# Performance work log

Measured on AMD Instinct MI355X. Metric: run time of the kernel, lower is better.

## Reference

```python
import jax, jax.numpy as jnp
import numpy as np

_SHAPE = (4, 2, 8, 256, 513)  # N, 2(real/imag), C, T, F


def setup_inputs() -> dict:
    key = jax.random.key(0)
    k1, k2, k3 = jax.random.split(key, 3)
    return {
        "mixture": jax.random.normal(k1, _SHAPE, dtype=jnp.float32),
        "target": jax.random.normal(k2, _SHAPE, dtype=jnp.float32),
        "noise": jax.random.normal(k3, _SHAPE, dtype=jnp.float32),
        "ref_mic_idx": 0,
    }


def _to_complex(x):
    # (N, 2, C, T, F) real-imag stacked -> complex (N, C, T, F)
    return jax.lax.complex(x[:, 0], x[:, 1])


def _mean_spatial_cov(s):
    # s: complex (N, C, T, F) -> time-averaged covariance (N, F, C, C)
    N, C, T, F = s.shape
    sc = jnp.transpose(s, (0, 3, 2, 1))  # (N, F, T, C)
    # outer product V V^H summed over T, fused into one batched GEMM
    return jnp.einsum("nftc,nftd->nfcd", sc, jnp.conj(sc)) / T


def reference(mixture, target, noise, ref_mic_idx):
    y = _to_complex(mixture)  # (N, C, T, F)
    x = _to_complex(target)
    v = _to_complex(noise)
    N, C, T, F = y.shape

    phi_target = _mean_spatial_cov(x)  # (N, F, C, C)
    # diagonal loading: torch adds load to BOTH real and imag parts (RI dim broadcast)
    load = (0.001 / np.sqrt(2)) * (1.0 + 1.0j)
    phi_noise = _mean_spatial_cov(v) + jnp.asarray(load, dtype=y.dtype) * jnp.eye(C, dtype=y.dtype)

    G = jnp.linalg.inv(phi_noise) @ phi_target  # (N, F, C, C)
    l = jnp.trace(G, axis1=-2, axis2=-1)  # (N, F)
    # W = (1/l) * G @ e_ref  -> select column ref_mic_idx
    W = G[..., ref_mic_idx] / l[..., None]  # (N, F, C)

    # X_bf(n,t,f) = W^H y = sum_c conj(W)_{nfc} y_{nctf}
    X_bf = jnp.einsum("nfc,nctf->ntf", jnp.conj(W), y)  # (N, T, F)
    # restack real/imag and add singleton channel dim -> (N, 2, 1, T, F)
    out = jnp.stack([X_bf.real, X_bf.imag], axis=1)[:, :, None]
    return out
```

## Files before the change

### kernel.cpp

```cpp
#include <hip/hip_runtime.h>

#define Nn 4
#define Cc 8
#define Tt 256
#define Ff 513
#define TFs (Tt * Ff)
#define NCHUNK 32
#define TCHUNK (Tt / NCHUNK)
#define SLAB ((size_t)Ff * 72)

__global__ __launch_bounds__(64) void cov_partial(
    const float* __restrict__ target, const float* __restrict__ noise,
    float* __restrict__ partial)
{
    int f = blockIdx.x * 64 + threadIdx.x;
    if (f >= Ff) return;
    int n = blockIdx.y;
    int z = blockIdx.z;
    int inp = z & 1;
    int chunk = z >> 1;

    const float* src = inp ? noise : target;
    const float* bt = src + (size_t)n * 2 * Cc * TFs + (size_t)(chunk * TCHUNK) * Ff + f;

    float ar[36], ai[36];
#pragma unroll
    for (int p = 0; p < 36; ++p) { ar[p] = 0.f; ai[p] = 0.f; }

#pragma unroll 2
    for (int tt = 0; tt < TCHUNK; ++tt) {
        float re[8], im[8];
#pragma unroll
        for (int c = 0; c < 8; ++c) {
            re[c] = bt[(size_t)c * TFs];
            im[c] = bt[(size_t)(Cc + c) * TFs];
        }
        int p = 0;
#pragma unroll
        for (int a = 0; a < 8; ++a) {
#pragma unroll
            for (int b = a; b < 8; ++b, ++p) {
                ar[p] += re[a] * re[b] + im[a] * im[b];
                if (a != b)
                    ai[p] += im[a] * re[b] - re[a] * im[b];
            }
        }
        bt += Ff;
    }

    float* dst = partial + (((size_t)inp * Nn + n) * NCHUNK + chunk) * SLAB
                 + (size_t)f * 72;
#pragma unroll
    for (int j = 0; j < 18; ++j) {
        float4 v = make_float4(ar[2 * j], ai[2 * j], ar[2 * j + 1], ai[2 * j + 1]);
        *(float4*)(dst + 4 * j) = v;
    }
}

__global__ __launch_bounds__(64) void mvdr_weights(
    const float* __restrict__ partial, const int* __restrict__ ref_ptr,
    float2* __restrict__ wconj)
{
    int f = blockIdx.x;
    int n = blockIdx.y;
    int lane = threadIdx.x;

    int r = lane >> 3, c = lane & 7;
    int lo = r < c ? r : c, hi = r < c ? c : r;
    int p = lo * 8 - lo * (lo - 1) / 2 + (hi - lo);

    const float* pT = partial + ((size_t)(0 * Nn + n) * NCHUNK) * SLAB
                      + (size_t)f * 72 + 2 * p;
    const float* pN = partial + ((size_t)(1 * Nn + n) * NCHUNK) * SLAB
                      + (size_t)f * 72 + 2 * p;
    float2 sT = make_float2(0.f, 0.f), sN = make_float2(0.f, 0.f);
#pragma unroll
    for (int ch = 0; ch < NCHUNK; ++ch) {
        float2 vT = *(const float2*)(pT + ch * SLAB);
        float2 vN = *(const float2*)(pN + ch * SLAB);
        sT.x += vT.x; sT.y += vT.y;
        sN.x += vN.x; sN.y += vN.y;
    }

    const float invT = 1.0f / (float)Tt;
    const float dl = 0.001f / 1.41421356237309515f;
    float sgn = (r > c) ? -1.f : 1.f;

    float2 a = make_float2(sN.x * invT, sgn * sN.y * invT);
    float2 b = make_float2(sT.x * invT, sgn * sT.y * invT);
    if (r == c) { a.x += dl; a.y += dl; }

    for (int k = 0; k < 8; ++k) {
        float mag = (c == k && r >= k) ? (a.x * a.x + a.y * a.y) : -1.f;
        int midx = r;
#pragma unroll
        for (int st = 8; st < 64; st <<= 1) {
            float om = __shfl_xor(mag, st, 64);
            int   oi = __shfl_xor(midx, st, 64);
            if (om > mag) { mag = om; midx = oi; }
        }
        int piv = __shfl(midx, k, 64);

        int srcr = (r == k) ? piv : ((r == piv) ? k : r);
        int src = srcr * 8 + c;
        a.x = __shfl(a.x, src, 64); a.y = __shfl(a.y, src, 64);
        b.x = __shfl(b.x, src, 64); b.y = __shfl(b.y, src, 64);

        float pvx = __shfl(a.x, k * 8 + k, 64), pvy = __shfl(a.y, k * 8 + k, 64);
        float d = pvx * pvx + pvy * pvy;
        float ipx = pvx / d, ipy = -pvy / d;
        if (r == k) {
            float2 t = a;
            a = make_float2(t.x * ipx - t.y * ipy, t.x * ipy + t.y * ipx);
            t = b;
            b = make_float2(t.x * ipx - t.y * ipy, t.x * ipy + t.y * ipx);
        }

        float rax = __shfl(a.x, k * 8 + c, 64), ray = __shfl(a.y, k * 8 + c, 64);
        float rbx = __shfl(b.x, k * 8 + c, 64), rby = __shfl(b.y, k * 8 + c, 64);
        float fx  = __shfl(a.x, r * 8 + k, 64), fy  = __shfl(a.y, r * 8 + k, 64);
        if (r != k) {
            a.x -= fx * rax - fy * ray;  a.y -= fx * ray + fy * rax;
            b.x -= fx * rbx - fy * rby;  b.y -= fx * rby + fy * rbx;
        }
    }

    float tx = (r == c) ? b.x : 0.f, ty = (r == c) ? b.y : 0.f;
#pragma unroll
    for (int st = 1; st < 64; st <<= 1) {
        tx += __shfl_xor(tx, st, 64);
        ty += __shfl_xor(ty, st, 64);
    }

    int ref = *ref_ptr;
    if (c == ref) {
        float den = tx * tx + ty * ty;
        float wx = (b.x * tx + b.y * ty) / den;
        float wy = (b.y * tx - b.x * ty) / den;
        wconj[((size_t)n * Ff + f) * 8 + r] = make_float2(wx, -wy);
    }
}

__global__ __launch_bounds__(256) void beamform(
    const float* __restrict__ y, const float2* __restrict__ wconj,
    float* __restrict__ out)
{
    int idx = blockIdx.x * 256 + threadIdx.x;
    int n = idx / TFs;
    int rem = idx - n * TFs;
    int t = rem / Ff;
    int f = rem - t * Ff;

    size_t base_re = (size_t)n * 2 * Cc * TFs + (size_t)t * Ff + f;
    size_t base_im = base_re + (size_t)Cc * TFs;
    const float2* w = wconj + ((size_t)n * Ff + f) * 8;

    float xr = 0.f, xi = 0.f;
#pragma unroll
    for (int c = 0; c < Cc; ++c) {
        float yre = y[base_re + (size_t)c * TFs];
        float yim = y[base_im + (size_t)c * TFs];
        float2 wc = w[c];
        xr += wc.x * yre - wc.y * yim;
        xi += wc.x * yim + wc.y * yre;
    }
    size_t ob = (size_t)n * 2 * TFs + (size_t)t * Ff + f;
    out[ob] = xr;
    out[ob + TFs] = xi;
}

extern "C" void kernel_launch(void* const* d_in, const int* in_sizes, int n_in,
                              void* d_out, int out_size, void* d_ws, size_t ws_size,
                              hipStream_t stream) {
    const float* mixture = (const float*)d_in[0];
    const float* target  = (const float*)d_in[1];
    const float* noise   = (const float*)d_in[2];
    const int*   refp    = (const int*)d_in[3];
    float* out = (float*)d_out;

    float*  partial = (float*)d_ws;
    float2* wconj = (float2*)((char*)d_ws +
                              (size_t)2 * Nn * NCHUNK * SLAB * sizeof(float));

    cov_partial<<<dim3(9, Nn, NCHUNK * 2), 64, 0, stream>>>(target, noise, partial);
    mvdr_weights<<<dim3(Ff, Nn), 64, 0, stream>>>(partial, refp, wconj);
    beamform<<<dim3((Nn * TFs) / 256), 256, 0, stream>>>(mixture, wconj, out);
}
```

Measured before the change: 156.8 us.

## Split covariance time chunk across four waves with LDS reduction and coalesced stores

Covariance partial blocks now hold four waves, each accumulating four time steps of a 16-step chunk, which halves the number of chunks and so the partial buffer. Waves combine their results through shared memory, and the per-block slab is written with contiguous, coalesced stores instead of strided float4 writes. mvdr_weights then reads half as many partials. The trade-off is extra shared-memory traffic, two barriers, and higher LDS use per block (about 37 KB).

After: 143.9 us. 1.09x faster.

```diff
diff --git a/kernel.cpp b/kernel.cpp
--- a/kernel.cpp
+++ b/kernel.cpp
@@ -5,30 +5,34 @@
 #define Tt 256
 #define Ff 513
 #define TFs (Tt * Ff)
-#define NCHUNK 32
+#define NCHUNK 16
 #define TCHUNK (Tt / NCHUNK)
 #define SLAB ((size_t)Ff * 72)
 
-__global__ __launch_bounds__(64) void cov_partial(
+__global__ __launch_bounds__(256) void cov_partial(
     const float* __restrict__ target, const float* __restrict__ noise,
     float* __restrict__ partial)
 {
-    int f = blockIdx.x * 64 + threadIdx.x;
-    if (f >= Ff) return;
+    int tid = threadIdx.x;
+    int lane = tid & 63, wave = tid >> 6;
+    int f0 = blockIdx.x * 64;
+    int f = f0 + lane;
+    int fc = f < Ff ? f : (Ff - 1);
     int n = blockIdx.y;
     int z = blockIdx.z;
     int inp = z & 1;
     int chunk = z >> 1;
 
     const float* src = inp ? noise : target;
-    const float* bt = src + (size_t)n * 2 * Cc * TFs + (size_t)(chunk * TCHUNK) * Ff + f;
+    const float* bt = src + (size_t)n * 2 * Cc * TFs
+                      + (size_t)(chunk * TCHUNK + wave * 4) * Ff + fc;
 
     float ar[36], ai[36];
 #pragma unroll
     for (int p = 0; p < 36; ++p) { ar[p] = 0.f; ai[p] = 0.f; }
 
 #pragma unroll 2
-    for (int tt = 0; tt < TCHUNK; ++tt) {
+    for (int tt = 0; tt < 4; ++tt) {
         float re[8], im[8];
 #pragma unroll
         for (int c = 0; c < 8; ++c) {
@@ -48,12 +52,37 @@
         bt += Ff;
     }
 
+    __shared__ float red[2][64][73];
+    int reg = wave & 1;
+    if (wave < 2) {
+        int p = 0;
+#pragma unroll
+        for (int a = 0; a < 8; ++a)
+#pragma unroll
+            for (int b = a; b < 8; ++b, ++p) {
+                red[reg][lane][2 * p]     = ar[p];
+                red[reg][lane][2 * p + 1] = (a == b) ? 0.f : ai[p];
+            }
+    }
+    __syncthreads();
+    if (wave >= 2) {
+        int p = 0;
+#pragma unroll
+        for (int a = 0; a < 8; ++a)
+#pragma unroll
+            for (int b = a; b < 8; ++b, ++p) {
+                red[reg][lane][2 * p] += ar[p];
+                if (a != b) red[reg][lane][2 * p + 1] += ai[p];
+            }
+    }
+    __syncthreads();
+
+    int nf = Ff - f0; if (nf > 64) nf = 64;
     float* dst = partial + (((size_t)inp * Nn + n) * NCHUNK + chunk) * SLAB
-                 + (size_t)f * 72;
-#pragma unroll
-    for (int j = 0; j < 18; ++j) {
-        float4 v = make_float4(ar[2 * j], ai[2 * j], ar[2 * j + 1], ai[2 * j + 1]);
-        *(float4*)(dst + 4 * j) = v;
+                 + (size_t)f0 * 72;
+    for (int i = tid; i < nf * 72; i += 256) {
+        int fl = i / 72, j = i - fl * 72;
+        dst[i] = red[0][fl][j] + red[1][fl][j];
     }
 }
 
@@ -182,7 +211,7 @@
     float2* wconj = (float2*)((char*)d_ws +
                               (size_t)2 * Nn * NCHUNK * SLAB * sizeof(float));
 
-    cov_partial<<<dim3(9, Nn, NCHUNK * 2), 64, 0, stream>>>(target, noise, partial);
+    cov_partial<<<dim3(9, Nn, NCHUNK * 2), 256, 0, stream>>>(target, noise, partial);
     mvdr_weights<<<dim3(Ff, Nn), 64, 0, stream>>>(partial, refp, wconj);
     beamform<<<dim3((Nn * TFs) / 256), 256, 0, stream>>>(mixture, wconj, out);
 }
```
